# Kernel optimization log

Measured on AMD Instinct MI355X. Metric: run time of the kernel, lower is better.

## Reference

```python
import jax, jax.numpy as jnp
import numpy as np

B, N, M, K, C = 4, 8192, 2048, 32, 64
RADIUS = 0.4
XYZ_OUT = 16  # xyz_mlps spec [3, 16]


def _mlp1(x, W, b):
    # SharedMLP layer: 1x1 Conv2d + ReLU (bn=False -> bias=True)
    return jax.nn.relu(jnp.einsum('oi,bimk->bomk', W, x) + b[None, :, None, None])


def _ball_query(xyz, new_xyz):
    # xyz: [B,N,3], new_xyz: [B,M,3] -> idx [B,M,K] int32, idn [B,M,K] {0,1}
    d2 = jnp.sum((new_xyz[:, :, None, :] - xyz[:, None, :, :]) ** 2, axis=-1)  # [B,M,N]
    within = d2 < RADIUS * RADIUS
    score = jnp.where(within, jnp.arange(N, dtype=jnp.int32), jnp.int32(N))
    neg, _ = jax.lax.top_k(-score, K)  # first K in-ball indices (ascending)
    idx = -neg
    valid = idx < N
    idx = jnp.where(valid, idx, idx[..., :1])  # pad with first neighbor (CUDA ball_query semantics)
    idx = jnp.clip(idx, 0, N - 1)
    return idx, valid.astype(jnp.int32)


def setup_inputs() -> dict:
    key = jax.random.key(0)
    ks = jax.random.split(key, 16)
    s = 0.1
    return {
        'xyz': jax.random.uniform(ks[0], (B, N, 3), jnp.float32),
        'new_xyz': jax.random.uniform(ks[1], (B, M, 3), jnp.float32),
        'features': jax.random.normal(ks[2], (B, C, N), jnp.float32),
        'query_features': jax.random.normal(ks[3], (B, C, M), jnp.float32),
        # query_feats_mlps[0]: [query_ch -> neigh_ch]
        'qW': s * jax.random.normal(ks[4], (C, C), jnp.float32),
        'qb': jnp.zeros((C,), jnp.float32),
        # ad_feats_mlps[0]: [neigh_ch -> neigh_ch]
        'afW': s * jax.random.normal(ks[5], (C, C), jnp.float32),
        'afb': jnp.zeros((C,), jnp.float32),
        # ad_xyz_mlps[0]: [3 -> neigh_ch]
        'axW': s * jax.random.normal(ks[6], (C, 3), jnp.float32),
        'axb': jnp.zeros((C,), jnp.float32),
        # mlps[0]: [64 -> 64 -> 64]
        'mW1': s * jax.random.normal(ks[7], (C, C), jnp.float32),
        'mb1': jnp.zeros((C,), jnp.float32),
        'mW2': s * jax.random.normal(ks[8], (C, C), jnp.float32),
        'mb2': jnp.zeros((C,), jnp.float32),
        # xyz_mlps[0]: [3 -> 16]
        'xW': s * jax.random.normal(ks[9], (XYZ_OUT, 3), jnp.float32),
        'xb': jnp.zeros((XYZ_OUT,), jnp.float32),
    }


def reference(xyz, new_xyz, features, query_features,
              qW, qb, afW, afb, axW, axb, mW1, mb1, mW2, mb2, xW, xb):
    idx, idn = _ball_query(xyz, new_xyz)  # [B,M,K]

    # gather neighbor xyz and features
    flat = idx.reshape(B, M * K)
    g_xyz = jnp.take_along_axis(xyz, flat[:, :, None], axis=1).reshape(B, M, K, 3)
    g_xyz = (g_xyz - new_xyz[:, :, None, :]).transpose(0, 3, 1, 2)  # [B,3,M,K] relative coords
    g_feat = jnp.take_along_axis(features, flat[:, None, :], axis=2).reshape(B, C, M, K)

    idn_mask = (jnp.sum(idn, axis=2) > 0).astype(jnp.float32)[:, :, None]  # [B,M,1]
    # _idn: rows with at least one neighbor keep idn, empty rows become all-ones
    _idn = jnp.where(idn_mask > 0, idn.astype(jnp.float32), 1.0)[:, None, :, :]  # [B,1,M,K]

    q = _mlp1(query_features[:, :, :, None], qW, qb)  # [B,C,M,1]

    feats_dist = _mlp1(q - g_feat, afW, afb)          # [B,C,M,K]
    space_dist = _mlp1(g_xyz, axW, axb)               # [B,C,M,K]
    bi_edge = feats_dist * space_dist

    dist = jnp.linalg.norm(g_xyz, axis=1, keepdims=True)  # [B,1,M,K]
    dist_recip = 1.0 / (dist + 1e-8)
    dist_recip = dist_recip / _idn
    norm = jnp.sum(dist_recip, axis=3, keepdims=True)
    weights = dist_recip / norm
    weights = weights * idn_mask[:, None, :, :]  # [B,1,M,K] * [B,1,M,1]

    nf = _mlp1(_mlp1(g_feat, mW1, mb1), mW2, mb2)  # [B,C,M,K]
    nf = weights * nf * bi_edge
    nf = jnp.sum(nf, axis=3)  # [B,C,M]

    nx = _mlp1(g_xyz, xW, xb)        # [B,16,M,K]
    nx = jnp.max(nx, axis=3)         # max_pool over neighbors -> [B,16,M]

    out = jnp.concatenate([nx, nf], axis=1)  # [B,80,M]
    return (new_xyz, out)
```

## Files before the change

### kernel.cpp

```cpp
#include <hip/hip_runtime.h>

#define B_ 4
#define N_ 8192
#define M_ 2048
#define K_ 32
#define R2 0.16f

__device__ __forceinline__ float readlane_f(float v, int k) {
  return __int_as_float(__builtin_amdgcn_readlane(__float_as_int(v), k));
}

__global__ __launch_bounds__(256) void prep(
    const float* __restrict__ feats, const float* __restrict__ qfeat,
    const float* __restrict__ qW, const float* __restrict__ qb,
    const float* __restrict__ afW, const float* __restrict__ afb,
    const float* __restrict__ mW1, const float* __restrict__ mb1,
    const float* __restrict__ mW2, const float* __restrict__ mb2,
    const float* __restrict__ new_xyz,
    float* __restrict__ PH, float* __restrict__ QA, float* __restrict__ outhead) {
  __shared__ float xt[64][65];
  __shared__ float x2[64][65];
  int b = blockIdx.y;
  int t = threadIdx.x, lane = t & 63;
  int g = __builtin_amdgcn_readfirstlane(t >> 6);

  if (blockIdx.x < N_ / 64) {
    int p0 = blockIdx.x * 64;
    const float* src = feats + ((size_t)b * 64 + g * 16) * N_ + p0 + lane;
#pragma unroll
    for (int cc = 0; cc < 16; ++cc) xt[g * 16 + cc][lane] = src[(size_t)cc * N_];
    __syncthreads();
    float pa[16];
    {
#pragma unroll
      for (int cc = 0; cc < 16; ++cc) pa[cc] = 0.0f;
#pragma unroll 4
      for (int i = 0; i < 64; ++i) {
        float xv = xt[i][lane];
#pragma unroll
        for (int cc = 0; cc < 16; ++cc) pa[cc] = fmaf(afW[(g * 16 + cc) * 64 + i], xv, pa[cc]);
      }
    }
    {
      float acc[16];
#pragma unroll
      for (int cc = 0; cc < 16; ++cc) acc[cc] = mb1[g * 16 + cc];
#pragma unroll 4
      for (int i = 0; i < 64; ++i) {
        float xv = xt[i][lane];
#pragma unroll
        for (int cc = 0; cc < 16; ++cc) acc[cc] = fmaf(mW1[(g * 16 + cc) * 64 + i], xv, acc[cc]);
      }
#pragma unroll
      for (int cc = 0; cc < 16; ++cc) x2[g * 16 + cc][lane] = fmaxf(acc[cc], 0.0f);
    }
    __syncthreads();
    {
      float h2[16];
#pragma unroll
      for (int cc = 0; cc < 16; ++cc) h2[cc] = mb2[g * 16 + cc];
#pragma unroll 4
      for (int i = 0; i < 64; ++i) {
        float xv = x2[i][lane];
#pragma unroll
        for (int cc = 0; cc < 16; ++cc) h2[cc] = fmaf(mW2[(g * 16 + cc) * 64 + i], xv, h2[cc]);
      }
      float4* o = (float4*)(PH + ((size_t)b * N_ + p0 + lane) * 128 + g * 32);
#pragma unroll
      for (int qd = 0; qd < 8; ++qd)
        o[qd] = make_float4(pa[2 * qd], fmaxf(h2[2 * qd], 0.0f),
                            pa[2 * qd + 1], fmaxf(h2[2 * qd + 1], 0.0f));
    }
  } else {
    int p0 = (blockIdx.x - N_ / 64) * 64;
    const float* src = qfeat + ((size_t)b * 64 + g * 16) * M_ + p0 + lane;
#pragma unroll
    for (int cc = 0; cc < 16; ++cc) xt[g * 16 + cc][lane] = src[(size_t)cc * M_];
    if (t < 192) {
      size_t o = (size_t)(b * M_ + p0) * 3 + t;
      outhead[o] = new_xyz[o];
    }
    __syncthreads();
    {
      float acc[16];
#pragma unroll
      for (int cc = 0; cc < 16; ++cc) acc[cc] = qb[g * 16 + cc];
#pragma unroll 4
      for (int i = 0; i < 64; ++i) {
        float xv = xt[i][lane];
#pragma unroll
        for (int cc = 0; cc < 16; ++cc) acc[cc] = fmaf(qW[(g * 16 + cc) * 64 + i], xv, acc[cc]);
      }
#pragma unroll
      for (int cc = 0; cc < 16; ++cc) x2[g * 16 + cc][lane] = fmaxf(acc[cc], 0.0f);
    }
    __syncthreads();
    {
      float acc[16];
#pragma unroll
      for (int cc = 0; cc < 16; ++cc) acc[cc] = afb[g * 16 + cc];
#pragma unroll 4
      for (int i = 0; i < 64; ++i) {
        float xv = x2[i][lane];
#pragma unroll
        for (int cc = 0; cc < 16; ++cc) acc[cc] = fmaf(afW[(g * 16 + cc) * 64 + i], xv, acc[cc]);
      }
      float4* o = (float4*)(QA + ((size_t)b * M_ + p0 + lane) * 64 + g * 16);
#pragma unroll
      for (int q = 0; q < 4; ++q)
        o[q] = make_float4(acc[4 * q], acc[4 * q + 1], acc[4 * q + 2], acc[4 * q + 3]);
    }
  }
}

__global__ __launch_bounds__(256) void grouper_main(
    const float* __restrict__ xyz, const float* __restrict__ new_xyz,
    const float* __restrict__ PH, const float* __restrict__ QA,
    const float* __restrict__ axW, const float* __restrict__ axb,
    const float* __restrict__ xW, const float* __restrict__ xb,
    float* __restrict__ out) {
  int wid = (int)((blockIdx.x * (size_t)blockDim.x + threadIdx.x) >> 6);
  int lane = threadIdx.x & 63;
  int b = wid >> 11;
  int m = wid & (M_ - 1);
  const float* qc = new_xyz + ((size_t)b * M_ + m) * 3;
  float cx = qc[0], cy = qc[1], cz = qc[2];
  const float* xbp = xyz + (size_t)b * N_ * 3;

  int idxreg = N_ - 1;
  float gxr = 0.f, gyr = 0.f, gzr = 0.f, d2r = 0.f;
  int cnt = 0;
  for (int base = 0; base < N_; base += 64) {
    int n = base + lane;
    const float* pp = xbp + 3 * n;
    float dx = pp[0] - cx, dy = pp[1] - cy, dz = pp[2] - cz;
    float d2 = dx * dx + dy * dy + dz * dz;
    bool inball = d2 < R2;
    unsigned long long mask = __ballot(inball);
    int pop = __popcll(mask);
    int before = __builtin_amdgcn_mbcnt_hi((unsigned)(mask >> 32),
                 __builtin_amdgcn_mbcnt_lo((unsigned)mask, 0));
    int pos = cnt + before;
    bool push = inball && (pos < K_);
    int dest = (push ? pos : 63) << 2;
    int rI = __builtin_amdgcn_ds_permute(dest, n);
    int rX = __builtin_amdgcn_ds_permute(dest, __float_as_int(dx));
    int rY = __builtin_amdgcn_ds_permute(dest, __float_as_int(dy));
    int rZ = __builtin_amdgcn_ds_permute(dest, __float_as_int(dz));
    int rD = __builtin_amdgcn_ds_permute(dest, __float_as_int(d2));
    int newcnt = cnt + pop;
    if ((lane >= cnt) && (lane < min(newcnt, K_))) {
      idxreg = rI; gxr = __int_as_float(rX); gyr = __int_as_float(rY);
      gzr = __int_as_float(rZ); d2r = __int_as_float(rD);
    }
    cnt = newcnt;
    if (cnt >= K_) break;
  }
  int nneigh = min(cnt, K_);
  if (nneigh == 0) {
    const float* pp = xbp + 3 * (N_ - 1);
    float dx = pp[0] - cx, dy = pp[1] - cy, dz = pp[2] - cz;
    if (lane == 0) {
      idxreg = N_ - 1; gxr = dx; gyr = dy; gzr = dz;
      d2r = dx * dx + dy * dy + dz * dz;
    }
  }
  int padn = max(nneigh, 1);
  {
    int i0 = __shfl(idxreg, 0);
    float x0 = __shfl(gxr, 0), y0 = __shfl(gyr, 0), z0 = __shfl(gzr, 0), d0 = __shfl(d2r, 0);
    if (lane >= padn) { idxreg = i0; gxr = x0; gyr = y0; gzr = z0; d2r = d0; }
  }
  float idn_mask = (nneigh > 0) ? 1.0f : 0.0f;

  float rslot = __builtin_amdgcn_rcpf(__builtin_amdgcn_sqrtf(d2r) + 1e-8f);
  if (nneigh > 0 && lane >= nneigh && lane < K_) rslot = __builtin_huge_valf();
  float Rsum;
  {
    float s = (lane < K_) ? rslot : 0.0f;
    s += __shfl_xor(s, 1);  s += __shfl_xor(s, 2);  s += __shfl_xor(s, 4);
    s += __shfl_xor(s, 8);  s += __shfl_xor(s, 16); s += __shfl_xor(s, 32);
    Rsum = s;
  }

  size_t qb64 = ((size_t)b * M_ + m) * 64;
  float QAm = QA[qb64 + lane];
  float ax0 = axW[lane * 3 + 0], ax1 = axW[lane * 3 + 1], ax2 = axW[lane * 3 + 2];
  float axbv = axb[lane];
  float xw0 = 0.f, xw1 = 0.f, xw2 = 0.f, xbv = 0.f;
  if (lane < 16) { xw0 = xW[lane * 3 + 0]; xw1 = xW[lane * 3 + 1]; xw2 = xW[lane * 3 + 2]; xbv = xb[lane]; }

  const float* PHb = PH + (size_t)b * N_ * 128;

  float accS = 0.f, nxmax = 0.f;
#pragma unroll
  for (int kg = 0; kg < 4; ++kg) {
    float2 v[8];
    float gxs[8], gys[8], gzs[8], rs[8];
#pragma unroll
    for (int j = 0; j < 8; ++j) {
      int k = kg * 8 + j;
      int n = __builtin_amdgcn_readlane(idxreg, k);
      gxs[j] = readlane_f(gxr, k);
      gys[j] = readlane_f(gyr, k);
      gzs[j] = readlane_f(gzr, k);
      rs[j]  = readlane_f(rslot, k);
      v[j] = *(const float2*)(PHb + (size_t)n * 128 + lane * 2);
    }
#pragma unroll
    for (int j = 0; j < 8; ++j) {
      float pa = v[j].x, h2 = v[j].y;
      float fd = fmaxf(QAm - pa, 0.f);
      float sd = fmaxf(fmaf(ax0, gxs[j], fmaf(ax1, gys[j], fmaf(ax2, gzs[j], axbv))), 0.f);
      accS = fmaf(rs[j], h2 * fd * sd, accS);
      float nv = fmaxf(fmaf(xw0, gxs[j], fmaf(xw1, gys[j], fmaf(xw2, gzs[j], xbv))), 0.f);
      nxmax = fmaxf(nxmax, nv);
    }
  }
  float nf = (accS / Rsum) * idn_mask;
  float* ob = out + (size_t)b * 80 * M_;
  ob[(size_t)(16 + lane) * M_ + m] = nf;
  if (lane < 16) ob[(size_t)lane * M_ + m] = nxmax;
}

extern "C" void kernel_launch(void* const* d_in, const int* in_sizes, int n_in,
                              void* d_out, int out_size, void* d_ws, size_t ws_size,
                              hipStream_t stream) {
  const float* xyz   = (const float*)d_in[0];
  const float* nxyz  = (const float*)d_in[1];
  const float* feats = (const float*)d_in[2];
  const float* qfeat = (const float*)d_in[3];
  const float* qW  = (const float*)d_in[4];
  const float* qb  = (const float*)d_in[5];
  const float* afW = (const float*)d_in[6];
  const float* afb = (const float*)d_in[7];
  const float* axW = (const float*)d_in[8];
  const float* axb = (const float*)d_in[9];
  const float* mW1 = (const float*)d_in[10];
  const float* mb1 = (const float*)d_in[11];
  const float* mW2 = (const float*)d_in[12];
  const float* mb2 = (const float*)d_in[13];
  const float* xW  = (const float*)d_in[14];
  const float* xb  = (const float*)d_in[15];

  float* ws = (float*)d_ws;
  size_t off = 0;
  float* PH = ws + off; off += (size_t)B_ * N_ * 128;
  float* QA = ws + off; off += (size_t)B_ * M_ * 64;
  if (ws_size < off * sizeof(float)) return;

  float* outhead = (float*)d_out;
  prep<<<dim3(N_ / 64 + M_ / 64, B_), 256, 0, stream>>>(
      feats, qfeat, qW, qb, afW, afb, mW1, mb1, mW2, mb2, nxyz, PH, QA, outhead);

  float* out_main = (float*)d_out + (size_t)B_ * M_ * 3;
  grouper_main<<<B_ * M_ / 4, 256, 0, stream>>>(xyz, nxyz, PH, QA,
                                                axW, axb, xW, xb, out_main);
}
```

Measured before the change: 136.7 us.

## Prefetch next xyz chunk in ball query, swizzle blocks, batch gather loads

Result: no change. 138.4 us (+1.2%).

```diff
diff --git a/kernel.cpp b/kernel.cpp
--- a/kernel.cpp
+++ b/kernel.cpp
@@ -119,7 +119,9 @@
     const float* __restrict__ axW, const float* __restrict__ axb,
     const float* __restrict__ xW, const float* __restrict__ xb,
     float* __restrict__ out) {
-  int wid = (int)((blockIdx.x * (size_t)blockDim.x + threadIdx.x) >> 6);
+  int bid = blockIdx.x;
+  int newbid = (bid & 7) * (int)(gridDim.x >> 3) + (bid >> 3);
+  int wid = newbid * 4 + (threadIdx.x >> 6);
   int lane = threadIdx.x & 63;
   int b = wid >> 11;
   int m = wid & (M_ - 1);
@@ -127,13 +129,30 @@
   float cx = qc[0], cy = qc[1], cz = qc[2];
   const float* xbp = xyz + (size_t)b * N_ * 3;
 
+  size_t qb64 = ((size_t)b * M_ + m) * 64;
+  float QAm = QA[qb64 + lane];
+  float ax0 = axW[lane * 3 + 0], ax1 = axW[lane * 3 + 1], ax2 = axW[lane * 3 + 2];
+  float axbv = axb[lane];
+  float xw0 = 0.f, xw1 = 0.f, xw2 = 0.f, xbv = 0.f;
+  if (lane < 16) { xw0 = xW[lane * 3 + 0]; xw1 = xW[lane * 3 + 1]; xw2 = xW[lane * 3 + 2]; xbv = xb[lane]; }
+
   int idxreg = N_ - 1;
   float gxr = 0.f, gyr = 0.f, gzr = 0.f, d2r = 0.f;
   int cnt = 0;
-  for (int base = 0; base < N_; base += 64) {
-    int n = base + lane;
-    const float* pp = xbp + 3 * n;
-    float dx = pp[0] - cx, dy = pp[1] - cy, dz = pp[2] - cz;
+  float c0, c1, c2;
+  {
+    const float* pp = xbp + 3 * lane;
+    c0 = pp[0]; c1 = pp[1]; c2 = pp[2];
+  }
+  int base = 0;
+  while (true) {
+    bool more = (base + 64) < N_;
+    float n0 = 0.f, n1 = 0.f, n2 = 0.f;
+    if (more) {
+      const float* pn = xbp + 3 * (base + 64 + lane);
+      n0 = pn[0]; n1 = pn[1]; n2 = pn[2];
+    }
+    float dx = c0 - cx, dy = c1 - cy, dz = c2 - cz;
     float d2 = dx * dx + dy * dy + dz * dz;
     bool inball = d2 < R2;
     unsigned long long mask = __ballot(inball);
@@ -143,6 +162,7 @@
     int pos = cnt + before;
     bool push = inball && (pos < K_);
     int dest = (push ? pos : 63) << 2;
+    int n = base + lane;
     int rI = __builtin_amdgcn_ds_permute(dest, n);
     int rX = __builtin_amdgcn_ds_permute(dest, __float_as_int(dx));
     int rY = __builtin_amdgcn_ds_permute(dest, __float_as_int(dy));
@@ -154,7 +174,8 @@
       gzr = __int_as_float(rZ); d2r = __int_as_float(rD);
     }
     cnt = newcnt;
-    if (cnt >= K_) break;
+    if (cnt >= K_ || !more) break;
+    base += 64; c0 = n0; c1 = n1; c2 = n2;
   }
   int nneigh = min(cnt, K_);
   if (nneigh == 0) {
@@ -183,41 +204,35 @@
     Rsum = s;
   }
 
-  size_t qb64 = ((size_t)b * M_ + m) * 64;
-  float QAm = QA[qb64 + lane];
-  float ax0 = axW[lane * 3 + 0], ax1 = axW[lane * 3 + 1], ax2 = axW[lane * 3 + 2];
-  float axbv = axb[lane];
-  float xw0 = 0.f, xw1 = 0.f, xw2 = 0.f, xbv = 0.f;
-  if (lane < 16) { xw0 = xW[lane * 3 + 0]; xw1 = xW[lane * 3 + 1]; xw2 = xW[lane * 3 + 2]; xbv = xb[lane]; }
-
   const float* PHb = PH + (size_t)b * N_ * 128;
 
-  float accS = 0.f, nxmax = 0.f;
-#pragma unroll
-  for (int kg = 0; kg < 4; ++kg) {
-    float2 v[8];
-    float gxs[8], gys[8], gzs[8], rs[8];
-#pragma unroll
-    for (int j = 0; j < 8; ++j) {
-      int k = kg * 8 + j;
-      int n = __builtin_amdgcn_readlane(idxreg, k);
-      gxs[j] = readlane_f(gxr, k);
-      gys[j] = readlane_f(gyr, k);
-      gzs[j] = readlane_f(gzr, k);
-      rs[j]  = readlane_f(rslot, k);
-      v[j] = *(const float2*)(PHb + (size_t)n * 128 + lane * 2);
-    }
-#pragma unroll
-    for (int j = 0; j < 8; ++j) {
-      float pa = v[j].x, h2 = v[j].y;
-      float fd = fmaxf(QAm - pa, 0.f);
-      float sd = fmaxf(fmaf(ax0, gxs[j], fmaf(ax1, gys[j], fmaf(ax2, gzs[j], axbv))), 0.f);
-      accS = fmaf(rs[j], h2 * fd * sd, accS);
-      float nv = fmaxf(fmaf(xw0, gxs[j], fmaf(xw1, gys[j], fmaf(xw2, gzs[j], xbv))), 0.f);
+  float accS0 = 0.f, accS1 = 0.f, nxmax = 0.f;
+#pragma unroll
+  for (int kg = 0; kg < 2; ++kg) {
+    int ns[16];
+    float2 v[16];
+#pragma unroll
+    for (int j = 0; j < 16; ++j)
+      ns[j] = __builtin_amdgcn_readlane(idxreg, kg * 16 + j);
+#pragma unroll
+    for (int j = 0; j < 16; ++j)
+      v[j] = *(const float2*)(PHb + (size_t)ns[j] * 128 + lane * 2);
+#pragma unroll
+    for (int j = 0; j < 16; ++j) {
+      int k = kg * 16 + j;
+      float gx = readlane_f(gxr, k);
+      float gy = readlane_f(gyr, k);
+      float gz = readlane_f(gzr, k);
+      float rr = readlane_f(rslot, k);
+      float fd = fmaxf(QAm - v[j].x, 0.f);
+      float sd = fmaxf(fmaf(ax0, gx, fmaf(ax1, gy, fmaf(ax2, gz, axbv))), 0.f);
+      float term = rr * (v[j].y * fd * sd);
+      if (j & 1) accS1 += term; else accS0 += term;
+      float nv = fmaxf(fmaf(xw0, gx, fmaf(xw1, gy, fmaf(xw2, gz, xbv))), 0.f);
       nxmax = fmaxf(nxmax, nv);
     }
   }
-  float nf = (accS / Rsum) * idn_mask;
+  float nf = ((accS0 + accS1) / Rsum) * idn_mask;
   float* ob = out + (size_t)b * 80 * M_;
   ob[(size_t)(16 + lane) * M_ + m] = nf;
   if (lane < 16) ob[(size_t)lane * M_ + m] = nxmax;
```

## Fuse prep and grouper into one persistent kernel with a grid barrier

Applied to the files above, without the earlier changes.

Result: slower. 469.5 us (+243.4%).

```diff
diff --git a/kernel.cpp b/kernel.cpp
--- a/kernel.cpp
+++ b/kernel.cpp
@@ -5,27 +5,33 @@
 #define M_ 2048
 #define K_ 32
 #define R2 0.16f
+#define GRID_ 1024
+#define POISON_ 0xAAAAAAAAu
 
 __device__ __forceinline__ float readlane_f(float v, int k) {
   return __int_as_float(__builtin_amdgcn_readlane(__float_as_int(v), k));
 }
 
-__global__ __launch_bounds__(256) void prep(
+__global__ __launch_bounds__(256, 4) void grouper_fused(
+    const float* __restrict__ xyz, const float* __restrict__ new_xyz,
     const float* __restrict__ feats, const float* __restrict__ qfeat,
     const float* __restrict__ qW, const float* __restrict__ qb,
     const float* __restrict__ afW, const float* __restrict__ afb,
+    const float* __restrict__ axW, const float* __restrict__ axb,
     const float* __restrict__ mW1, const float* __restrict__ mb1,
     const float* __restrict__ mW2, const float* __restrict__ mb2,
-    const float* __restrict__ new_xyz,
-    float* __restrict__ PH, float* __restrict__ QA, float* __restrict__ outhead) {
+    const float* __restrict__ xW, const float* __restrict__ xb,
+    float* __restrict__ PH, float* __restrict__ QA,
+    unsigned* __restrict__ ctr,
+    float* __restrict__ outhead, float* __restrict__ out) {
   __shared__ float xt[64][65];
   __shared__ float x2[64][65];
-  int b = blockIdx.y;
+  int blk = blockIdx.x;
   int t = threadIdx.x, lane = t & 63;
   int g = __builtin_amdgcn_readfirstlane(t >> 6);
 
-  if (blockIdx.x < N_ / 64) {
-    int p0 = blockIdx.x * 64;
+  if (blk < 512) {
+    int b = blk >> 7, p0 = (blk & 127) * 64;
     const float* src = feats + ((size_t)b * 64 + g * 16) * N_ + p0 + lane;
 #pragma unroll
     for (int cc = 0; cc < 16; ++cc) xt[g * 16 + cc][lane] = src[(size_t)cc * N_];
@@ -51,6 +57,7 @@
 #pragma unroll
         for (int cc = 0; cc < 16; ++cc) acc[cc] = fmaf(mW1[(g * 16 + cc) * 64 + i], xv, acc[cc]);
       }
+      __syncthreads();
 #pragma unroll
       for (int cc = 0; cc < 16; ++cc) x2[g * 16 + cc][lane] = fmaxf(acc[cc], 0.0f);
     }
@@ -71,8 +78,9 @@
         o[qd] = make_float4(pa[2 * qd], fmaxf(h2[2 * qd], 0.0f),
                             pa[2 * qd + 1], fmaxf(h2[2 * qd + 1], 0.0f));
     }
-  } else {
-    int p0 = (blockIdx.x - N_ / 64) * 64;
+  } else if (blk < 640) {
+    int qi = blk - 512;
+    int b = qi >> 5, p0 = (qi & 31) * 64;
     const float* src = qfeat + ((size_t)b * 64 + g * 16) * M_ + p0 + lane;
 #pragma unroll
     for (int cc = 0; cc < 16; ++cc) xt[g * 16 + cc][lane] = src[(size_t)cc * M_];
@@ -91,6 +99,7 @@
 #pragma unroll
         for (int cc = 0; cc < 16; ++cc) acc[cc] = fmaf(qW[(g * 16 + cc) * 64 + i], xv, acc[cc]);
       }
+      __syncthreads();
 #pragma unroll
       for (int cc = 0; cc < 16; ++cc) x2[g * 16 + cc][lane] = fmaxf(acc[cc], 0.0f);
     }
@@ -111,116 +120,125 @@
         o[q] = make_float4(acc[4 * q], acc[4 * q + 1], acc[4 * q + 2], acc[4 * q + 3]);
     }
   }
-}
-
-__global__ __launch_bounds__(256) void grouper_main(
-    const float* __restrict__ xyz, const float* __restrict__ new_xyz,
-    const float* __restrict__ PH, const float* __restrict__ QA,
-    const float* __restrict__ axW, const float* __restrict__ axb,
-    const float* __restrict__ xW, const float* __restrict__ xb,
-    float* __restrict__ out) {
-  int wid = (int)((blockIdx.x * (size_t)blockDim.x + threadIdx.x) >> 6);
-  int lane = threadIdx.x & 63;
-  int b = wid >> 11;
-  int m = wid & (M_ - 1);
-  const float* qc = new_xyz + ((size_t)b * M_ + m) * 3;
-  float cx = qc[0], cy = qc[1], cz = qc[2];
-  const float* xbp = xyz + (size_t)b * N_ * 3;
-
-  int idxreg = N_ - 1;
-  float gxr = 0.f, gyr = 0.f, gzr = 0.f, d2r = 0.f;
-  int cnt = 0;
-  for (int base = 0; base < N_; base += 64) {
-    int n = base + lane;
-    const float* pp = xbp + 3 * n;
-    float dx = pp[0] - cx, dy = pp[1] - cy, dz = pp[2] - cz;
-    float d2 = dx * dx + dy * dy + dz * dz;
-    bool inball = d2 < R2;
-    unsigned long long mask = __ballot(inball);
-    int pop = __popcll(mask);
-    int before = __builtin_amdgcn_mbcnt_hi((unsigned)(mask >> 32),
-                 __builtin_amdgcn_mbcnt_lo((unsigned)mask, 0));
-    int pos = cnt + before;
-    bool push = inball && (pos < K_);
-    int dest = (push ? pos : 63) << 2;
-    int rI = __builtin_amdgcn_ds_permute(dest, n);
-    int rX = __builtin_amdgcn_ds_permute(dest, __float_as_int(dx));
-    int rY = __builtin_amdgcn_ds_permute(dest, __float_as_int(dy));
-    int rZ = __builtin_amdgcn_ds_permute(dest, __float_as_int(dz));
-    int rD = __builtin_amdgcn_ds_permute(dest, __float_as_int(d2));
-    int newcnt = cnt + pop;
-    if ((lane >= cnt) && (lane < min(newcnt, K_))) {
-      idxreg = rI; gxr = __int_as_float(rX); gyr = __int_as_float(rY);
-      gzr = __int_as_float(rZ); d2r = __int_as_float(rD);
-    }
-    cnt = newcnt;
-    if (cnt >= K_) break;
+
+  __threadfence();
+  __syncthreads();
+  if (t == 0) {
+    atomicCAS(ctr, POISON_, 0u);
+    atomicAdd(ctr, 1u);
+    int guard = 0;
+    while (__hip_atomic_load(ctr, __ATOMIC_ACQUIRE, __HIP_MEMORY_SCOPE_AGENT) < (unsigned)GRID_ &&
+           ++guard < (1 << 24))
+      __builtin_amdgcn_s_sleep(2);
   }
-  int nneigh = min(cnt, K_);
-  if (nneigh == 0) {
-    const float* pp = xbp + 3 * (N_ - 1);
-    float dx = pp[0] - cx, dy = pp[1] - cy, dz = pp[2] - cz;
-    if (lane == 0) {
-      idxreg = N_ - 1; gxr = dx; gyr = dy; gzr = dz;
-      d2r = dx * dx + dy * dy + dz * dz;
-    }
-  }
-  int padn = max(nneigh, 1);
-  {
-    int i0 = __shfl(idxreg, 0);
-    float x0 = __shfl(gxr, 0), y0 = __shfl(gyr, 0), z0 = __shfl(gzr, 0), d0 = __shfl(d2r, 0);
-    if (lane >= padn) { idxreg = i0; gxr = x0; gyr = y0; gzr = z0; d2r = d0; }
-  }
-  float idn_mask = (nneigh > 0) ? 1.0f : 0.0f;
-
-  float rslot = __builtin_amdgcn_rcpf(__builtin_amdgcn_sqrtf(d2r) + 1e-8f);
-  if (nneigh > 0 && lane >= nneigh && lane < K_) rslot = __builtin_huge_valf();
-  float Rsum;
-  {
-    float s = (lane < K_) ? rslot : 0.0f;
-    s += __shfl_xor(s, 1);  s += __shfl_xor(s, 2);  s += __shfl_xor(s, 4);
-    s += __shfl_xor(s, 8);  s += __shfl_xor(s, 16); s += __shfl_xor(s, 32);
-    Rsum = s;
-  }
-
-  size_t qb64 = ((size_t)b * M_ + m) * 64;
-  float QAm = QA[qb64 + lane];
+  __syncthreads();
+  __threadfence();
+
   float ax0 = axW[lane * 3 + 0], ax1 = axW[lane * 3 + 1], ax2 = axW[lane * 3 + 2];
   float axbv = axb[lane];
   float xw0 = 0.f, xw1 = 0.f, xw2 = 0.f, xbv = 0.f;
   if (lane < 16) { xw0 = xW[lane * 3 + 0]; xw1 = xW[lane * 3 + 1]; xw2 = xW[lane * 3 + 2]; xbv = xb[lane]; }
 
-  const float* PHb = PH + (size_t)b * N_ * 128;
-
-  float accS = 0.f, nxmax = 0.f;
-#pragma unroll
-  for (int kg = 0; kg < 4; ++kg) {
-    float2 v[8];
-    float gxs[8], gys[8], gzs[8], rs[8];
-#pragma unroll
-    for (int j = 0; j < 8; ++j) {
-      int k = kg * 8 + j;
-      int n = __builtin_amdgcn_readlane(idxreg, k);
-      gxs[j] = readlane_f(gxr, k);
-      gys[j] = readlane_f(gyr, k);
-      gzs[j] = readlane_f(gzr, k);
-      rs[j]  = readlane_f(rslot, k);
-      v[j] = *(const float2*)(PHb + (size_t)n * 128 + lane * 2);
-    }
-#pragma unroll
-    for (int j = 0; j < 8; ++j) {
-      float pa = v[j].x, h2 = v[j].y;
-      float fd = fmaxf(QAm - pa, 0.f);
-      float sd = fmaxf(fmaf(ax0, gxs[j], fmaf(ax1, gys[j], fmaf(ax2, gzs[j], axbv))), 0.f);
-      accS = fmaf(rs[j], h2 * fd * sd, accS);
-      float nv = fmaxf(fmaf(xw0, gxs[j], fmaf(xw1, gys[j], fmaf(xw2, gzs[j], xbv))), 0.f);
-      nxmax = fmaxf(nxmax, nv);
-    }
+  int newbid = (blk & 7) * (GRID_ / 8) + (blk >> 3);
+  int wavebase = newbid * 4 + (t >> 6);
+
+#pragma unroll 1
+  for (int rep = 0; rep < 2; ++rep) {
+    int wid = wavebase * 2 + rep;
+    int b = wid >> 11;
+    int m = wid & (M_ - 1);
+    const float* qc = new_xyz + ((size_t)b * M_ + m) * 3;
+    float cx = qc[0], cy = qc[1], cz = qc[2];
+    const float* xbp = xyz + (size_t)b * N_ * 3;
+    size_t qb64 = ((size_t)b * M_ + m) * 64;
+    float QAm = QA[qb64 + lane];
+
+    int idxreg = N_ - 1;
+    float gxr = 0.f, gyr = 0.f, gzr = 0.f, d2r = 0.f;
+    int cnt = 0;
+    for (int base = 0; base < N_; base += 64) {
+      int n = base + lane;
+      const float* pp = xbp + 3 * n;
+      float dx = pp[0] - cx, dy = pp[1] - cy, dz = pp[2] - cz;
+      float d2 = dx * dx + dy * dy + dz * dz;
+      bool inball = d2 < R2;
+      unsigned long long mask = __ballot(inball);
+      int pop = __popcll(mask);
+      int before = __builtin_amdgcn_mbcnt_hi((unsigned)(mask >> 32),
+                   __builtin_amdgcn_mbcnt_lo((unsigned)mask, 0));
+      int pos = cnt + before;
+      bool push = inball && (pos < K_);
+      int dest = (push ? pos : 63) << 2;
+      int rI = __builtin_amdgcn_ds_permute(dest, n);
+      int rX = __builtin_amdgcn_ds_permute(dest, __float_as_int(dx));
+      int rY = __builtin_amdgcn_ds_permute(dest, __float_as_int(dy));
+      int rZ = __builtin_amdgcn_ds_permute(dest, __float_as_int(dz));
+      int rD = __builtin_amdgcn_ds_permute(dest, __float_as_int(d2));
+      int newcnt = cnt + pop;
+      if ((lane >= cnt) && (lane < min(newcnt, K_))) {
+        idxreg = rI; gxr = __int_as_float(rX); gyr = __int_as_float(rY);
+        gzr = __int_as_float(rZ); d2r = __int_as_float(rD);
+      }
+      cnt = newcnt;
+      if (cnt >= K_) break;
+    }
+    int nneigh = min(cnt, K_);
+    if (nneigh == 0) {
+      const float* pp = xbp + 3 * (N_ - 1);
+      float dx = pp[0] - cx, dy = pp[1] - cy, dz = pp[2] - cz;
+      if (lane == 0) {
+        idxreg = N_ - 1; gxr = dx; gyr = dy; gzr = dz;
+        d2r = dx * dx + dy * dy + dz * dz;
+      }
+    }
+    int padn = max(nneigh, 1);
+    {
+      int i0 = __shfl(idxreg, 0);
+      float x0 = __shfl(gxr, 0), y0 = __shfl(gyr, 0), z0 = __shfl(gzr, 0), d0 = __shfl(d2r, 0);
+      if (lane >= padn) { idxreg = i0; gxr = x0; gyr = y0; gzr = z0; d2r = d0; }
+    }
+    float idn_mask = (nneigh > 0) ? 1.0f : 0.0f;
+
+    float rslot = __builtin_amdgcn_rcpf(__builtin_amdgcn_sqrtf(d2r) + 1e-8f);
+    if (nneigh > 0 && lane >= nneigh && lane < K_) rslot = __builtin_huge_valf();
+    float Rsum;
+    {
+      float s = (lane < K_) ? rslot : 0.0f;
+      s += __shfl_xor(s, 1);  s += __shfl_xor(s, 2);  s += __shfl_xor(s, 4);
+      s += __shfl_xor(s, 8);  s += __shfl_xor(s, 16); s += __shfl_xor(s, 32);
+      Rsum = s;
+    }
+
+    const float* PHb = PH + (size_t)b * N_ * 128;
+    float accS = 0.f, nxmax = 0.f;
+#pragma unroll
+    for (int kg = 0; kg < 4; ++kg) {
+      float2 v[8];
+      float gxs[8], gys[8], gzs[8], rs[8];
+#pragma unroll
+      for (int j = 0; j < 8; ++j) {
+        int k = kg * 8 + j;
+        int n = __builtin_amdgcn_readlane(idxreg, k);
+        gxs[j] = readlane_f(gxr, k);
+        gys[j] = readlane_f(gyr, k);
+        gzs[j] = readlane_f(gzr, k);
+        rs[j]  = readlane_f(rslot, k);
+        v[j] = *(const float2*)(PHb + (size_t)n * 128 + lane * 2);
+      }
+#pragma unroll
+      for (int j = 0; j < 8; ++j) {
+        float fd = fmaxf(QAm - v[j].x, 0.f);
+        float sd = fmaxf(fmaf(ax0, gxs[j], fmaf(ax1, gys[j], fmaf(ax2, gzs[j], axbv))), 0.f);
+        accS = fmaf(rs[j], v[j].y * fd * sd, accS);
+        float nv = fmaxf(fmaf(xw0, gxs[j], fmaf(xw1, gys[j], fmaf(xw2, gzs[j], xbv))), 0.f);
+        nxmax = fmaxf(nxmax, nv);
+      }
+    }
+    float nf = (accS / Rsum) * idn_mask;
+    float* ob = out + (size_t)b * 80 * M_;
+    ob[(size_t)(16 + lane) * M_ + m] = nf;
+    if (lane < 16) ob[(size_t)lane * M_ + m] = nxmax;
   }
-  float nf = (accS / Rsum) * idn_mask;
-  float* ob = out + (size_t)b * 80 * M_;
-  ob[(size_t)(16 + lane) * M_ + m] = nf;
-  if (lane < 16) ob[(size_t)lane * M_ + m] = nxmax;
 }
 
 extern "C" void kernel_launch(void* const* d_in, const int* in_sizes, int n_in,
@@ -247,13 +265,13 @@
   size_t off = 0;
   float* PH = ws + off; off += (size_t)B_ * N_ * 128;
   float* QA = ws + off; off += (size_t)B_ * M_ * 64;
+  unsigned* ctr = (unsigned*)(ws + off); off += 32;
   if (ws_size < off * sizeof(float)) return;
 
   float* outhead = (float*)d_out;
-  prep<<<dim3(N_ / 64 + M_ / 64, B_), 256, 0, stream>>>(
-      feats, qfeat, qW, qb, afW, afb, mW1, mb1, mW2, mb2, nxyz, PH, QA, outhead);
-
   float* out_main = (float*)d_out + (size_t)B_ * M_ * 3;
-  grouper_main<<<B_ * M_ / 4, 256, 0, stream>>>(xyz, nxyz, PH, QA,
-                                                axW, axb, xW, xb, out_main);
+
+  grouper_fused<<<GRID_, 256, 0, stream>>>(
+      xyz, nxyz, feats, qfeat, qW, qb, afW, afb, axW, axb,
+      mW1, mb1, mW2, mb2, xW, xb, PH, QA, ctr, outhead, out_main);
 }
```
